# Kernel optimization log

Measured on AMD Instinct MI355X. Metric: run time of the kernel, lower is better.

The kernel has to match this reference:

```python
import jax, jax.numpy as jnp
import numpy as np

IDIM = 128
C = 3  # nb_sh_channels
S = 256  # nb_samples
R = 2048  # nb_rays

DELTA_IJK = jnp.array([(0, 0, 0), (1, 0, 0), (0, 1, 0), (1, 1, 0),
                       (0, 0, 1), (1, 0, 1), (0, 1, 1), (1, 1, 1)], dtype=jnp.int32)
K_SH = jnp.array([0.28209479, 0.48860251, 0.48860251, 0.48860251,
                  1.09254843, 1.09254843, 0.31539157, 1.09254843, 0.54627422],
                 dtype=jnp.float32)


def sh_cartesian(d):
    # real SH basis (degree <= 2) of unit direction, scaled by K_SH -> (R, 9)
    dn = d / jnp.linalg.norm(d, axis=-1, keepdims=True)
    x, y, z = dn[..., 0], dn[..., 1], dn[..., 2]
    basis = jnp.stack([jnp.ones_like(x), y, z, x,
                       x * y, y * z, 3.0 * z * z - 1.0, x * z, x * x - y * y], axis=-1)
    return basis * K_SH


def setup_inputs() -> dict:
    key = jax.random.key(0)
    ks = jax.random.split(key, 6)
    # origins inside [IDIM/4, 3*IDIM/4]^3 so samples never leave the box
    x = IDIM / 4.0 + jax.random.uniform(ks[0], (R, 3), jnp.float32) * (IDIM / 2.0)
    d = jax.random.normal(ks[1], (R, 3), jnp.float32)
    d = d / jnp.linalg.norm(d, axis=-1, keepdims=True)
    tmin = jnp.zeros((R,), jnp.float32)
    tmax = 1.0 + jax.random.uniform(ks[2], (R,), jnp.float32) * (IDIM / 8.0 - 1.0)
    u = jax.random.uniform(ks[3], (R, S), jnp.float32)  # the torch.rand samples
    grid = jax.random.uniform(ks[4], (IDIM, IDIM, IDIM, 9 * C), jnp.float32)
    opacity = jax.random.uniform(ks[5], (IDIM, IDIM, IDIM), jnp.float32)
    return {"x": x, "d": d, "tmin": tmin, "tmax": tmax, "u": u,
            "grid": grid, "opacity": opacity}


def reference(x, d, tmin, tmax, u, grid, opacity):
    nb_rays = x.shape[0]
    # stratified-random samples along each ray, sorted
    samples = (tmax[:, None] - tmin[:, None]) * u + tmin[:, None]
    samples = jnp.sort(samples, axis=1)                      # (R, S)
    # sample points and enclosing voxel (delta_voxel = [1,1,1])
    pts = x[:, None, :] + samples[:, :, None] * d[:, None, :]  # (R, S, 3)
    cell = jnp.clip(jnp.floor(pts).astype(jnp.int32), 0, IDIM - 2)
    frac = pts - cell.astype(pts.dtype)                       # (R, S, 3)
    idx = cell[:, :, None, :] + DELTA_IJK                     # (R, S, 8, 3)
    # trilinear weights matching DELTA_IJK corner ordering
    w = jnp.prod(jnp.where(DELTA_IJK == 1, frac[:, :, None, :], 1.0 - frac[:, :, None, :]),
                 axis=-1)                                     # (R, S, 8)
    gi = (idx[..., 0] * IDIM + idx[..., 1]) * IDIM + idx[..., 2]  # flat voxel id
    harms = grid.reshape(-1, 9 * C)[gi]                       # (R, S, 8, 9C) gather
    opac = opacity.reshape(-1)[gi]                            # (R, S, 8)   gather
    interp_sh = jnp.einsum('rse,rsec->rsc', w, harms)         # (R, S, 9C)
    interp_op = jnp.sum(w * opac, axis=-1)                    # (R, S)
    # SH shading
    sh = jnp.tile(sh_cartesian(d), (1, C))                    # (R, 9C)
    interp_harm = (interp_sh * sh[:, None, :]).reshape(nb_rays, S, C, 9)
    # volumetric compositing
    deltas = samples[:, 1:] - samples[:, :-1]                 # (R, S-1)
    dts = deltas * interp_op[:, :-1]
    cum = jnp.cumsum(dts, axis=1)
    cum = jnp.concatenate([jnp.zeros((nb_rays, 1), dts.dtype), cum[:, :-1]], axis=1)
    samples_color = jnp.clip(jnp.sum(interp_harm, axis=3) + 0.5, 0.0, None)  # (R, S, C)
    rays_color = jnp.sum(jnp.exp(-cum)[:, :, None] * (1.0 - jnp.exp(-dts))[:, :, None]
                         * samples_color[:, :-1, :], axis=1)  # (R, C)
    return rays_color
```

## Files before the change

kernel.cpp:

```cpp
#include <hip/hip_runtime.h>

#define IDIM 128
#define NS 256
#define NR 2048

__global__ __launch_bounds__(256)
void rf_kernel(const float* __restrict__ x, const float* __restrict__ dvec,
               const float* __restrict__ tmin, const float* __restrict__ tmax,
               const float* __restrict__ u, const float* __restrict__ grid,
               const float* __restrict__ opacity, float* __restrict__ out)
{
    const int ray = blockIdx.x;
    const int t = threadIdx.x;

    __shared__ float s_samp[NS];
    __shared__ float s_scan[NS];
    __shared__ float s_red[4][3];

    const float ox = x[ray*3+0], oy = x[ray*3+1], oz = x[ray*3+2];
    const float dx = dvec[ray*3+0], dy = dvec[ray*3+1], dz = dvec[ray*3+2];
    const float t0 = tmin[ray], t1 = tmax[ray];

    float samp = (t1 - t0) * u[ray*NS + t] + t0;
    s_samp[t] = samp;
    __syncthreads();

    for (int k = 2; k <= NS; k <<= 1) {
        for (int j = k >> 1; j > 0; j >>= 1) {
            int ixj = t ^ j;
            if (ixj > t) {
                float a = s_samp[t], b = s_samp[ixj];
                bool up = ((t & k) == 0);
                if ((a > b) == up) { s_samp[t] = b; s_samp[ixj] = a; }
            }
            __syncthreads();
        }
    }

    samp = s_samp[t];
    float samp_next = (t < NS-1) ? s_samp[t+1] : samp;

    const float rn = rsqrtf(dx*dx + dy*dy + dz*dz);
    const float sx = dx*rn, sy = dy*rn, sz = dz*rn;
    float sh[9];
    sh[0] = 0.28209479f;
    sh[1] = 0.48860251f * sy;
    sh[2] = 0.48860251f * sz;
    sh[3] = 0.48860251f * sx;
    sh[4] = 1.09254843f * sx*sy;
    sh[5] = 1.09254843f * sy*sz;
    sh[6] = 0.31539157f * (3.0f*sz*sz - 1.0f);
    sh[7] = 1.09254843f * sx*sz;
    sh[8] = 0.54627422f * (sx*sx - sy*sy);

    const float px = ox + samp*dx, py = oy + samp*dy, pz = oz + samp*dz;
    int ci = min(max((int)floorf(px), 0), IDIM-2);
    int cj = min(max((int)floorf(py), 0), IDIM-2);
    int ck = min(max((int)floorf(pz), 0), IDIM-2);
    const float fx = px - (float)ci, fy = py - (float)cj, fz = pz - (float)ck;

    float c0 = 0.f, c1 = 0.f, c2 = 0.f, op = 0.f;
    #pragma unroll
    for (int e = 0; e < 8; ++e) {
        const int di = e & 1, dj = (e >> 1) & 1, dk = (e >> 2) & 1;
        const float w = (di ? fx : 1.f - fx) * (dj ? fy : 1.f - fy) * (dk ? fz : 1.f - fz);
        const int gi = ((ci + di) * IDIM + (cj + dj)) * IDIM + (ck + dk);
        const float* __restrict__ g = grid + (long)gi * 27;
        float d0 = 0.f, d1 = 0.f, d2 = 0.f;
        #pragma unroll
        for (int q = 0; q < 9; ++q) {
            d0 += sh[q] * g[q];
            d1 += sh[q] * g[9 + q];
            d2 += sh[q] * g[18 + q];
        }
        c0 += w * d0; c1 += w * d1; c2 += w * d2;
        op += w * opacity[gi];
    }
    c0 = fmaxf(c0 + 0.5f, 0.f);
    c1 = fmaxf(c1 + 0.5f, 0.f);
    c2 = fmaxf(c2 + 0.5f, 0.f);

    const float dts = (t < NS-1) ? (samp_next - samp) * op : 0.f;

    s_scan[t] = dts;
    __syncthreads();
    for (int off = 1; off < NS; off <<= 1) {
        float v = (t >= off) ? s_scan[t - off] : 0.f;
        __syncthreads();
        s_scan[t] += v;
        __syncthreads();
    }
    const float cum = s_scan[t] - dts;

    const float wgt = (t < NS-1) ? expf(-cum) * (1.f - expf(-dts)) : 0.f;
    float r0 = wgt * c0, r1 = wgt * c1, r2 = wgt * c2;

    #pragma unroll
    for (int off = 32; off > 0; off >>= 1) {
        r0 += __shfl_down(r0, off);
        r1 += __shfl_down(r1, off);
        r2 += __shfl_down(r2, off);
    }
    const int lane = t & 63, wv = t >> 6;
    if (lane == 0) { s_red[wv][0] = r0; s_red[wv][1] = r1; s_red[wv][2] = r2; }
    __syncthreads();
    if (t == 0) {
        out[ray*3+0] = s_red[0][0] + s_red[1][0] + s_red[2][0] + s_red[3][0];
        out[ray*3+1] = s_red[0][1] + s_red[1][1] + s_red[2][1] + s_red[3][1];
        out[ray*3+2] = s_red[0][2] + s_red[1][2] + s_red[2][2] + s_red[3][2];
    }
}

extern "C" void kernel_launch(void* const* d_in, const int* in_sizes, int n_in,
                              void* d_out, int out_size, void* d_ws, size_t ws_size,
                              hipStream_t stream) {
    const float* x       = (const float*)d_in[0];
    const float* d       = (const float*)d_in[1];
    const float* tmin    = (const float*)d_in[2];
    const float* tmax    = (const float*)d_in[3];
    const float* u       = (const float*)d_in[4];
    const float* grid    = (const float*)d_in[5];
    const float* opacity = (const float*)d_in[6];
    float* out = (float*)d_out;
    rf_kernel<<<NR, NS, 0, stream>>>(x, d, tmin, tmax, u, grid, opacity, out);
}
```

Baseline: 303.6 us.

## Deduplicate voxel corner gathers per ray via shared-memory slots and warp-shuffle scan

Since sorted samples along a ray often fall in the same voxel, the kernel now finds unique consecutive cells with a ballot and prefix count. For up to 64 unique cells it computes the SH-projected corner values once, in parallel, and stores them in shared memory. Samples then interpolate from these shared corners, and any overflow falls back to the direct gather. The LDS-based scan is also replaced with a wavefront shuffle scan plus a cross-wave fixup. This cuts redundant global gathers and barriers, at the cost of extra syncs and shared memory use.

```diff
diff --git a/kernel.cpp b/kernel.cpp
--- a/kernel.cpp
+++ b/kernel.cpp
@@ -3,6 +3,7 @@
 #define IDIM 128
 #define NS 256
 #define NR 2048
+#define SLOTS 64
 
 __global__ __launch_bounds__(256)
 void rf_kernel(const float* __restrict__ x, const float* __restrict__ dvec,
@@ -12,10 +13,15 @@
 {
     const int ray = blockIdx.x;
     const int t = threadIdx.x;
+    const int lane = t & 63, wv = t >> 6;
 
-    __shared__ float s_samp[NS];
-    __shared__ float s_scan[NS];
-    __shared__ float s_red[4][3];
+    __shared__ float  s_samp[NS];
+    __shared__ int    s_key[NS];
+    __shared__ int    s_slotkey[SLOTS];
+    __shared__ int    s_wsum[4];
+    __shared__ float  s_wred[4];
+    __shared__ float4 s_corner[SLOTS][9];
+    __shared__ float  s_red[4][3];
 
     const float ox = x[ray*3+0], oy = x[ray*3+1], oz = x[ray*3+2];
     const float dx = dvec[ray*3+0], dy = dvec[ray*3+1], dz = dvec[ray*3+2];
@@ -38,7 +44,7 @@
     }
 
     samp = s_samp[t];
-    float samp_next = (t < NS-1) ? s_samp[t+1] : samp;
+    const float samp_next = (t < NS-1) ? s_samp[t+1] : samp;
 
     const float rn = rsqrtf(dx*dx + dy*dy + dz*dz);
     const float sx = dx*rn, sy = dy*rn, sz = dz*rn;
@@ -54,17 +60,35 @@
     sh[8] = 0.54627422f * (sx*sx - sy*sy);
 
     const float px = ox + samp*dx, py = oy + samp*dy, pz = oz + samp*dz;
-    int ci = min(max((int)floorf(px), 0), IDIM-2);
-    int cj = min(max((int)floorf(py), 0), IDIM-2);
-    int ck = min(max((int)floorf(pz), 0), IDIM-2);
+    const int ci = min(max((int)floorf(px), 0), IDIM-2);
+    const int cj = min(max((int)floorf(py), 0), IDIM-2);
+    const int ck = min(max((int)floorf(pz), 0), IDIM-2);
     const float fx = px - (float)ci, fy = py - (float)cj, fz = pz - (float)ck;
 
-    float c0 = 0.f, c1 = 0.f, c2 = 0.f, op = 0.f;
+    const int key = (ci << 14) | (cj << 7) | ck;
+    s_key[t] = key;
+    __syncthreads();
+    const bool leader = (t == 0) || (s_key[t-1] != key);
+    const unsigned long long m = __ballot(leader);
+    const int incl = __popcll(m & (~0ull >> (63 - lane)));
+    if (lane == 63) s_wsum[wv] = __popcll(m);
+    __syncthreads();
+    int base = 0;
     #pragma unroll
-    for (int e = 0; e < 8; ++e) {
-        const int di = e & 1, dj = (e >> 1) & 1, dk = (e >> 2) & 1;
-        const float w = (di ? fx : 1.f - fx) * (dj ? fy : 1.f - fy) * (dk ? fz : 1.f - fz);
-        const int gi = ((ci + di) * IDIM + (cj + dj)) * IDIM + (ck + dk);
+    for (int w = 0; w < 4; ++w) base += (w < wv) ? s_wsum[w] : 0;
+    const int slot = base + incl - 1;
+    const int U = s_wsum[0] + s_wsum[1] + s_wsum[2] + s_wsum[3];
+    if (leader && slot < SLOTS) s_slotkey[slot] = key;
+    __syncthreads();
+
+    const int Ucap = (U < SLOTS ? U : SLOTS);
+    for (int task = t; task < Ucap * 8; task += NS) {
+        const int sl = task >> 3, e = task & 7;
+        const int k2 = s_slotkey[sl];
+        const int bi = (k2 >> 14) + (e & 1);
+        const int bj = ((k2 >> 7) & 127) + ((e >> 1) & 1);
+        const int bk = (k2 & 127) + ((e >> 2) & 1);
+        const int gi = (bi * IDIM + bj) * IDIM + bk;
         const float* __restrict__ g = grid + (long)gi * 27;
         float d0 = 0.f, d1 = 0.f, d2 = 0.f;
         #pragma unroll
@@ -73,8 +97,39 @@
             d1 += sh[q] * g[9 + q];
             d2 += sh[q] * g[18 + q];
         }
-        c0 += w * d0; c1 += w * d1; c2 += w * d2;
-        op += w * opacity[gi];
+        s_corner[sl][e] = make_float4(d0, d1, d2, opacity[gi]);
+    }
+    __syncthreads();
+
+    float c0, c1, c2, op;
+    if (slot < SLOTS) {
+        c0 = c1 = c2 = op = 0.f;
+        #pragma unroll
+        for (int e = 0; e < 8; ++e) {
+            const float w = ((e & 1) ? fx : 1.f - fx)
+                          * (((e >> 1) & 1) ? fy : 1.f - fy)
+                          * (((e >> 2) & 1) ? fz : 1.f - fz);
+            const float4 v = s_corner[slot][e];
+            c0 += w * v.x; c1 += w * v.y; c2 += w * v.z; op += w * v.w;
+        }
+    } else {
+        c0 = c1 = c2 = op = 0.f;
+        for (int e = 0; e < 8; ++e) {
+            const float w = ((e & 1) ? fx : 1.f - fx)
+                          * (((e >> 1) & 1) ? fy : 1.f - fy)
+                          * (((e >> 2) & 1) ? fz : 1.f - fz);
+            const int gi = ((ci + (e & 1)) * IDIM + (cj + ((e >> 1) & 1))) * IDIM
+                         + (ck + ((e >> 2) & 1));
+            const float* __restrict__ g = grid + (long)gi * 27;
+            float d0 = 0.f, d1 = 0.f, d2 = 0.f;
+            for (int q = 0; q < 9; ++q) {
+                d0 += sh[q] * g[q];
+                d1 += sh[q] * g[9 + q];
+                d2 += sh[q] * g[18 + q];
+            }
+            c0 += w * d0; c1 += w * d1; c2 += w * d2;
+            op += w * opacity[gi];
+        }
     }
     c0 = fmaxf(c0 + 0.5f, 0.f);
     c1 = fmaxf(c1 + 0.5f, 0.f);
@@ -82,15 +137,18 @@
 
     const float dts = (t < NS-1) ? (samp_next - samp) * op : 0.f;
 
-    s_scan[t] = dts;
+    float v = dts;
+    #pragma unroll
+    for (int off = 1; off < 64; off <<= 1) {
+        const float n = __shfl_up(v, off);
+        if (lane >= off) v += n;
+    }
+    if (lane == 63) s_wred[wv] = v;
     __syncthreads();
-    for (int off = 1; off < NS; off <<= 1) {
-        float v = (t >= off) ? s_scan[t - off] : 0.f;
-        __syncthreads();
-        s_scan[t] += v;
-        __syncthreads();
-    }
-    const float cum = s_scan[t] - dts;
+    float wbase = 0.f;
+    #pragma unroll
+    for (int w = 0; w < 4; ++w) wbase += (w < wv) ? s_wred[w] : 0.f;
+    const float cum = (v + wbase) - dts;
 
     const float wgt = (t < NS-1) ? expf(-cum) * (1.f - expf(-dts)) : 0.f;
     float r0 = wgt * c0, r1 = wgt * c1, r2 = wgt * c2;
@@ -101,7 +159,6 @@
         r1 += __shfl_down(r1, off);
         r2 += __shfl_down(r2, off);
     }
-    const int lane = t & 63, wv = t >> 6;
     if (lane == 0) { s_red[wv][0] = r0; s_red[wv][1] = r1; s_red[wv][2] = r2; }
     __syncthreads();
     if (t == 0) {
```

Measured after the change: 283.9 us. 1.07x faster.
